# Optimization experiments

Measured on AMD Instinct MI355X. Metric: run time of the kernel, lower is better.

Reference implementation:

```python
import jax, jax.numpy as jnp
import numpy as np
import math

G, T, D, B = 20000, 1536, 512, 256
TOPK = 32


def setup_inputs() -> dict:
    key = jax.random.key(0)
    k1, k2, k3, k4 = jax.random.split(key, 4)
    tg_dec = jax.random.normal(k1, (G, D), dtype=jnp.float32)
    tf_base = jax.random.normal(k2, (T, D), dtype=jnp.float32)
    tf_expr = jax.random.normal(k3, (B, T), dtype=jnp.float32)
    motif_mask = jax.random.randint(k4, (G, T), 0, 2).astype(jnp.int32)
    scale = jnp.full((1,), 0.1, dtype=jnp.float32)  # nn.Parameter scale
    return {"tg_dec": tg_dec, "tf_base": tf_base, "tf_expr": tf_expr,
            "motif_mask": motif_mask, "scale": scale}


def reference(tg_dec, tf_base, tf_expr, motif_mask, scale):
    # scaled similarity: [G, T]
    sim = jnp.matmul(tg_dec, tf_base.T) / math.sqrt(tf_base.shape[1])
    # masked fill where motif prior is absent
    sim = jnp.where(motif_mask == 0, -jnp.inf, sim)
    attn = jax.nn.softmax(sim, axis=-1)
    attn = jnp.nan_to_num(attn, nan=0.0)
    # top-k selection + scatter mask + renormalize
    _, topk_idx = jax.lax.top_k(attn, TOPK)              # [G, TOPK]
    rows = jnp.arange(attn.shape[0])[:, None]
    mask = jnp.zeros_like(attn).at[rows, topk_idx].set(1.0)
    attn = attn * mask
    attn = attn / (attn.sum(axis=-1, keepdims=True) + 1e-8)
    # weighted combine: [B, G]
    tf_scalar = jnp.matmul(tf_expr, attn.T)
    # dropout is identity in eval mode
    return (scale[0] * tf_scalar, attn)
```

## Files before the change

### kernel.cpp

```cpp
#include <hip/hip_runtime.h>
#include <cstdint>

typedef unsigned short u16;
typedef unsigned int   u32;
typedef unsigned long long u64;

#define G_ROWS 20000
#define G_PAD  20096
#define T_DIM  1536
#define D_DIM  512
#define B_DIM  256
#define TOPK   32
#define SIM_SCALE 0.04419417382415922f
#define SQRT_D    22.62741699796952f
#define BOUND_EPS 2.0e-4f

typedef __bf16 bf16x8 __attribute__((ext_vector_type(8)));
typedef float  f32x4  __attribute__((ext_vector_type(4)));

__device__ __forceinline__ u16 f2bf(float f) {
  u32 u = __float_as_uint(f);
  u += 0x7fffu + ((u >> 16) & 1u);
  return (u16)(u >> 16);
}
__device__ __forceinline__ float bf2f(u16 h) {
  return __uint_as_float(((u32)h) << 16);
}
__device__ __forceinline__ u32 fkey(float v) {
  u32 b = __float_as_uint(v);
  return (b & 0x80000000u) ? ~b : (b | 0x80000000u);
}
__device__ __forceinline__ float funkey(u32 o) {
  u32 b = (o & 0x80000000u) ? (o & 0x7FFFFFFFu) : ~o;
  return __uint_as_float(b);
}

__global__ __launch_bounds__(256) void prep(const float* __restrict__ tg_dec,
                                            const float* __restrict__ tf_base,
                                            const float* __restrict__ tf_expr,
                                            u16* __restrict__ Ah, u16* __restrict__ Al,
                                            u16* __restrict__ Bh, u16* __restrict__ Bl,
                                            float* __restrict__ tfT)
{
  __shared__ float tile[32][33];
  const int b = blockIdx.x;
  const int tid = threadIdx.x;
  if (b < 10816) {
    const float* src; u16 *hi, *lo; int valid_rows; int bb;
    if (b < 10048) { src = tg_dec; hi = Ah; lo = Al; valid_rows = G_ROWS; bb = b; }
    else           { src = tf_base; hi = Bh; lo = Bl; valid_rows = T_DIM; bb = b - 10048; }
    size_t i = ((size_t)bb * 256 + tid) * 4;
    int row = (int)(i >> 9);
    float4 a = make_float4(0.f, 0.f, 0.f, 0.f);
    if (row < valid_rows) a = *(const float4*)(src + i);
    float v[4] = {a.x, a.y, a.z, a.w};
    u16 h[4], l[4];
#pragma unroll
    for (int c = 0; c < 4; ++c) {
      h[c] = f2bf(v[c]);
      l[c] = f2bf(v[c] - bf2f(h[c]));
    }
    *(uint2*)(hi + i) = make_uint2((u32)h[0] | ((u32)h[1] << 16), (u32)h[2] | ((u32)h[3] << 16));
    *(uint2*)(lo + i) = make_uint2((u32)l[0] | ((u32)l[1] << 16), (u32)l[2] | ((u32)l[3] << 16));
  } else {
    const int t = b - 10816;
    const int x = tid & 31, y = tid >> 5;
    const int bt = (t % 48) * 32;
    const int bb = (t / 48) * 32;
#pragma unroll
    for (int i = 0; i < 32; i += 8) tile[y + i][x] = tf_expr[(size_t)(bb + y + i) * T_DIM + bt + x];
    __syncthreads();
#pragma unroll
    for (int i = 0; i < 32; i += 8) tfT[(size_t)(bt + y + i) * B_DIM + bb + x] = tile[x][y + i];
  }
}

__device__ __forceinline__ void gl16(const u16* g, u16* l) {
  __builtin_amdgcn_global_load_lds((__attribute__((address_space(1))) void*)(void*)g,
                                   (__attribute__((address_space(3))) void*)l, 16, 0, 0);
}

#define NBX 6
#define NWG 474

__global__ __launch_bounds__(512, 2) void gemm_split(const u16* __restrict__ Ah, const u16* __restrict__ Al,
                                                     const u16* __restrict__ Bh, const u16* __restrict__ Bl,
                                                     float* __restrict__ Sim)
{
  __shared__ u16 sm[65536];

  const int orig = blockIdx.x;
  const int xcd  = orig & 7;
  const int q    = NWG >> 3, r = NWG & 7;
  const int wgid = (xcd < r ? xcd * (q + 1) : r * (q + 1) + (xcd - r) * q) + (orig >> 3);
  const int by   = wgid / NBX;
  const int bx   = wgid - by * NBX;
  const int bm0  = by * 256;
  const int bn0  = bx * 256;

  const int tid  = threadIdx.x;
  const int lane = tid & 63;
  const int wv   = tid >> 6;
  const int wm   = wv >> 2;
  const int wn   = wv & 3;
  const int la8  = lane << 3;

  const int sub  = wv << 1;
  const int srow = lane & 15;
  const int skc  = (lane >> 4) << 3;
  const u16* gA0 = Ah + (size_t)(bm0 + (sub + 0) * 16 + srow) * 512 + skc;
  const u16* gA1 = Ah + (size_t)(bm0 + (sub + 1) * 16 + srow) * 512 + skc;
  const u16* gAl0 = Al + (size_t)(bm0 + (sub + 0) * 16 + srow) * 512 + skc;
  const u16* gAl1 = Al + (size_t)(bm0 + (sub + 1) * 16 + srow) * 512 + skc;
  const u16* gB0 = Bh + (size_t)(bn0 + (sub + 0) * 16 + srow) * 512 + skc;
  const u16* gB1 = Bh + (size_t)(bn0 + (sub + 1) * 16 + srow) * 512 + skc;
  const u16* gBl0 = Bl + (size_t)(bn0 + (sub + 0) * 16 + srow) * 512 + skc;
  const u16* gBl1 = Bl + (size_t)(bn0 + (sub + 1) * 16 + srow) * 512 + skc;

#define STAGE_A(p, ktn) do {                                   \
    const size_t ko = (size_t)(ktn) << 5;                      \
    u16* d = sm + (p) * 16384 + sub * 512;                     \
    gl16(gA0 + ko,  d);                                        \
    gl16(gA1 + ko,  d + 512);                                  \
    gl16(gAl0 + ko, d + 8192);                                 \
    gl16(gAl1 + ko, d + 8192 + 512);                           \
  } while (0)
#define STAGE_B(p, ktn) do {                                   \
    const size_t ko = (size_t)(ktn) << 5;                      \
    u16* d = sm + 32768 + (p) * 16384 + sub * 512;             \
    gl16(gB0 + ko,  d);                                        \
    gl16(gB1 + ko,  d + 512);                                  \
    gl16(gBl0 + ko, d + 8192);                                 \
    gl16(gBl1 + ko, d + 8192 + 512);                           \
  } while (0)

  f32x4 acc[8][4];
#pragma unroll
  for (int i = 0; i < 8; ++i)
#pragma unroll
    for (int j = 0; j < 4; ++j) acc[i][j] = (f32x4){0.f, 0.f, 0.f, 0.f};

  bf16x8 aH[4], aL[4], bH[4], bL[4];

#define READ_A(rbA, half) do {                                                     \
    _Pragma("unroll")                                                              \
    for (int i = 0; i < 4; ++i) {                                                  \
      aH[i] = *(const bf16x8*)((rbA) + (wm * 8 + (half) * 4 + i) * 512 + la8);     \
      aL[i] = *(const bf16x8*)((rbA) + 8192 + (wm * 8 + (half) * 4 + i) * 512 + la8); \
    }                                                                              \
  } while (0)
#define READ_B(rbB, half) do {                                                     \
    _Pragma("unroll")                                                              \
    for (int i = 0; i < 2; ++i) {                                                  \
      bH[(half) * 2 + i] = *(const bf16x8*)((rbB) + (wn * 4 + (half) * 2 + i) * 512 + la8); \
      bL[(half) * 2 + i] = *(const bf16x8*)((rbB) + 8192 + (wn * 4 + (half) * 2 + i) * 512 + la8); \
    }                                                                              \
  } while (0)
#define MFMA_Q(qm, qn) do {                                                        \
    __builtin_amdgcn_s_setprio(1);                                                 \
    _Pragma("unroll")                                                              \
    for (int m2 = 0; m2 < 4; ++m2)                                                 \
      _Pragma("unroll")                                                            \
      for (int n2 = 0; n2 < 2; ++n2) {                                             \
        const int mi = (qm) * 4 + m2, ni = (qn) * 2 + n2;                          \
        acc[mi][ni] = __builtin_amdgcn_mfma_f32_16x16x32_bf16(aH[m2], bH[ni], acc[mi][ni], 0, 0, 0); \
        acc[mi][ni] = __builtin_amdgcn_mfma_f32_16x16x32_bf16(aH[m2], bL[ni], acc[mi][ni], 0, 0, 0); \
        acc[mi][ni] = __builtin_amdgcn_mfma_f32_16x16x32_bf16(aL[m2], bH[ni], acc[mi][ni], 0, 0, 0); \
      }                                                                            \
    __builtin_amdgcn_s_setprio(0);                                                 \
  } while (0)
#define LGKM0 do { asm volatile("s_waitcnt lgkmcnt(0)" ::: "memory"); __builtin_amdgcn_sched_barrier(0); } while (0)
#define BAR   do { __builtin_amdgcn_sched_barrier(0); __builtin_amdgcn_s_barrier(); } while (0)

  STAGE_A(0, 0);
  STAGE_B(0, 0);
  STAGE_A(1, 1);

#pragma unroll 2
  for (int kt = 0; kt < 16; ++kt) {
    const u16* rbA = sm + (kt & 1) * 16384;
    const u16* rbB = sm + 32768 + (kt & 1) * 16384;

    asm volatile("s_waitcnt vmcnt(4)" ::: "memory");
    BAR;
    READ_A(rbA, 0);
    READ_B(rbB, 0);
    LGKM0;
    MFMA_Q(0, 0);
    BAR;

    if (kt < 15) STAGE_B((kt + 1) & 1, kt + 1);
    READ_B(rbB, 1);
    LGKM0;
    MFMA_Q(0, 1);
    BAR;

    READ_A(rbA, 1);
    LGKM0;
    MFMA_Q(1, 0);
    BAR;

    if (kt < 14) STAGE_A(kt & 1, kt + 2);
    MFMA_Q(1, 1);
  }
#undef STAGE_A
#undef STAGE_B
#undef READ_A
#undef READ_B
#undef MFMA_Q
#undef LGKM0
#undef BAR

  const int erow0 = bm0 + (wm << 7) + ((lane >> 4) << 2);
  const int ecol0 = bn0 + (wn << 6) + (lane & 15);
#pragma unroll
  for (int mi = 0; mi < 8; ++mi)
#pragma unroll
    for (int rr = 0; rr < 4; ++rr) {
      int row = erow0 + mi * 16 + rr;
      if (row < G_ROWS) {
#pragma unroll
        for (int ni = 0; ni < 4; ++ni)
          Sim[(size_t)row * T_DIM + ecol0 + ni * 16] = acc[mi][ni][rr] * SIM_SCALE;
      }
    }
}

__device__ __forceinline__ int count_ge(const float* v, float tau) {
  int c = 0;
#pragma unroll
  for (int j = 0; j < 24; ++j) c += (int)__popcll(__ballot(v[j] >= tau));
  return c;
}
__device__ __forceinline__ u64 bitonic64_desc(u64 key, int lane) {
#pragma unroll
  for (int k = 2; k <= 64; k <<= 1) {
#pragma unroll
    for (int j = k >> 1; j > 0; j >>= 1) {
      u64 p = __shfl_xor(key, j, 64);
      bool lower = (lane & j) == 0;
      bool asc   = (lane & k) != 0;
      u64 mn = (key < p) ? key : p;
      u64 mx = (key < p) ? p : key;
      key = (lower == asc) ? mn : mx;
    }
  }
  return key;
}

__global__ __launch_bounds__(256) void topk_kernel(float* __restrict__ Sim, const int* __restrict__ mask,
                                                   const float* __restrict__ tg_dec,
                                                   const float* __restrict__ tf_base,
                                                   int* __restrict__ tIdx, float* __restrict__ tW)
{
  __shared__ u32 cval[4][64];
  __shared__ int cidxs[4][64];
  const int lane = threadIdx.x & 63;
  const int wv   = threadIdx.x >> 6;
  const int g    = blockIdx.x * 4 + wv;
  float* row = Sim + (size_t)g * T_DIM;
  const int* mrow = mask + (size_t)g * T_DIM;

  float v[24];
#pragma unroll
  for (int j = 0; j < 6; ++j) {
    float4 q = *(const float4*)(row + j * 256 + lane * 4);
    int4  mq = *(const int4*)(mrow + j * 256 + lane * 4);
    v[j * 4 + 0] = mq.x ? q.x : -INFINITY;
    v[j * 4 + 1] = mq.y ? q.y : -INFINITY;
    v[j * 4 + 2] = mq.z ? q.z : -INFINITY;
    v[j * 4 + 3] = mq.w ? q.w : -INFINITY;
  }

  const float TH0 = 1.25f, TH1 = 1.40f, TH2 = 1.55f, TH3 = 1.70f, TH4 = 1.85f, TH5 = 2.00f;
  int n0 = 0, n1 = 0, n2 = 0, n3 = 0, n4 = 0, n5 = 0, nv = 0;
#pragma unroll
  for (int j = 0; j < 24; ++j) {
    float x = v[j];
    n0 += (x >= TH0); n1 += (x >= TH1); n2 += (x >= TH2);
    n3 += (x >= TH3); n4 += (x >= TH4); n5 += (x >= TH5);
    nv += (x != -INFINITY);
  }
  u64 p0 = (u64)(u32)n0 | ((u64)(u32)n1 << 16) | ((u64)(u32)n2 << 32) | ((u64)(u32)n3 << 48);
  u64 p1 = (u64)(u32)n4 | ((u64)(u32)n5 << 16) | ((u64)(u32)nv << 32);
#pragma unroll
  for (int off = 32; off > 0; off >>= 1) {
    p0 += __shfl_xor(p0, off, 64);
    p1 += __shfl_xor(p1, off, 64);
  }
  int c[6];
  c[0] = (int)(p0 & 0xFFFF); c[1] = (int)((p0 >> 16) & 0xFFFF);
  c[2] = (int)((p0 >> 32) & 0xFFFF); c[3] = (int)((p0 >> 48) & 0xFFFF);
  c[4] = (int)(p1 & 0xFFFF); c[5] = (int)((p1 >> 16) & 0xFFFF);
  const int cvalid = (int)((p1 >> 32) & 0xFFFF);

  float tau; int cnt;
  if (cvalid <= 64) { tau = -3.0e38f; cnt = cvalid; }
  else {
    int is = -1;
#pragma unroll
    for (int i = 0; i < 6; ++i) if (c[i] >= 33) is = i;
    const float THv[7] = {TH0, TH1, TH2, TH3, TH4, TH5, 8.0f};
    if (is >= 0 && c[is] <= 64) { tau = THv[is]; cnt = c[is]; }
    else {
      float lo, hi;
      if (is < 0) { lo = -4.0f; hi = TH0; }
      else        { lo = THv[is]; hi = THv[is + 1]; }
      tau = lo; cnt = 1000;
      for (int it = 0; it < 16; ++it) {
        float mid = 0.5f * (lo + hi);
        int cm = count_ge(v, mid);
        if (cm > 64)      lo = mid;
        else if (cm < 33) hi = mid;
        else { tau = mid; cnt = cm; break; }
      }
      if (cnt == 1000) tau = lo;
    }
  }

  int base = 0;
#pragma unroll
  for (int j = 0; j < 24; ++j) {
    bool pred = (v[j] >= tau);
    u64 bmc = __ballot(pred);
    int pos = base + (int)__popcll(bmc & ((1ull << lane) - 1ull));
    int idx = (j >> 2) * 256 + lane * 4 + (j & 3);
    if (pred && pos < 64) { cval[wv][pos] = fkey(v[j]); cidxs[wv][pos] = idx; }
    base += (int)__popcll(bmc);
  }
  const int cnt_eff = (base < 64) ? base : 64;

  u64 key = 0;
  if (lane < cnt_eff)
    key = ((u64)cval[wv][lane] << 32) | (u64)(u32)(~(u32)cidxs[wv][lane]);

  key = bitonic64_desc(key, lane);
  int   myidx = (int)(~(u32)key);
  float myv   = (key != 0) ? funkey((u32)(key >> 32)) : -INFINITY;

  float v31 = __shfl(myv, 31, 64);
  float v32 = __shfl(myv, 32, 64);
  if (cnt_eff > TOPK && (v31 - v32) < 2.0f * BOUND_EPS) {
    bool flag = (lane < cnt_eff) &&
                (myv >= v32 - 2.0f * BOUND_EPS) && (myv <= v31 + 2.0f * BOUND_EPS);
    if (flag) {
      const float* arow_g = tg_dec + (size_t)g * D_DIM;
      const float* brow   = tf_base + (size_t)myidx * D_DIM;
      float s1 = 0.f, s2 = 0.f;
#pragma unroll 8
      for (int k = 0; k < 384; k += 4) {
        float4 av = *(const float4*)(arow_g + k);
        float4 bv = *(const float4*)(brow + k);
        s1 = fmaf(av.x, bv.x, s1); s1 = fmaf(av.y, bv.y, s1);
        s1 = fmaf(av.z, bv.z, s1); s1 = fmaf(av.w, bv.w, s1);
      }
#pragma unroll 8
      for (int k = 384; k < 512; k += 4) {
        float4 av = *(const float4*)(arow_g + k);
        float4 bv = *(const float4*)(brow + k);
        s2 = fmaf(av.x, bv.x, s2); s2 = fmaf(av.y, bv.y, s2);
        s2 = fmaf(av.z, bv.z, s2); s2 = fmaf(av.w, bv.w, s2);
      }
      myv = (s1 + s2) / SQRT_D;
      key = ((u64)fkey(myv) << 32) | (u64)(u32)(~(u32)myidx);
    }
    key = bitonic64_desc(key, lane);
    myidx = (int)(~(u32)key);
    myv   = (key != 0) ? funkey((u32)(key >> 32)) : -INFINITY;
  }

  const bool selme = (lane < TOPK) && (lane < cnt_eff);
  float mx = __shfl(myv, 0, 64);
  float e = selme ? __expf(myv - mx) : 0.f;
  float E = e;
#pragma unroll
  for (int off = 32; off > 0; off >>= 1) E += __shfl_xor(E, off, 64);
  float rden = (E > 0.f) ? (1.f / E) : 0.f;
  float w = e * rden;

  const float4 z4 = make_float4(0.f, 0.f, 0.f, 0.f);
#pragma unroll
  for (int j = 0; j < 6; ++j) *(float4*)(row + j * 256 + lane * 4) = z4;
  asm volatile("s_waitcnt vmcnt(0)" ::: "memory");
  if (selme) row[myidx] = w;

  if (cnt_eff < TOPK && lane >= cnt_eff && lane < TOPK) {
    tIdx[(size_t)g * TOPK + lane] = 0; tW[(size_t)g * TOPK + lane] = 0.f;
  }
  if (selme) {
    tIdx[(size_t)g * TOPK + lane] = myidx;
    tW[(size_t)g * TOPK + lane]   = w;
  }
}

__global__ __launch_bounds__(256) void combine_kernel(const float* __restrict__ tfT, const int* __restrict__ tIdx,
                                                      const float* __restrict__ tW, const float* __restrict__ scalep,
                                                      float* __restrict__ out0)
{
  __shared__ int   sIdx[16 * 32];
  __shared__ float sW[16 * 32];
  const int tid = threadIdx.x;
  const int g0 = blockIdx.x * 16;
  for (int i = tid; i < 512; i += 256) {
    sIdx[i] = tIdx[(size_t)g0 * 32 + i];
    sW[i]   = tW[(size_t)g0 * 32 + i];
  }
  __syncthreads();
  const float scale = scalep[0];
  float acc[16];
#pragma unroll
  for (int gi = 0; gi < 16; ++gi) acc[gi] = 0.f;
#pragma unroll 4
  for (int gi = 0; gi < 16; ++gi) {
    float a = 0.f;
#pragma unroll
    for (int k = 0; k < 32; ++k) {
      float w = sW[gi * 32 + k];
      int t   = sIdx[gi * 32 + k];
      a += w * tfT[(size_t)t * B_DIM + tid];
    }
    acc[gi] = a;
  }
  float* dst = out0 + (size_t)tid * G_ROWS + g0;
#pragma unroll
  for (int q = 0; q < 4; ++q) {
    float4 o = make_float4(scale * acc[4*q], scale * acc[4*q+1], scale * acc[4*q+2], scale * acc[4*q+3]);
    *(float4*)(dst + 4 * q) = o;
  }
}

extern "C" void kernel_launch(void* const* d_in, const int* in_sizes, int n_in,
                              void* d_out, int out_size, void* d_ws, size_t ws_size,
                              hipStream_t stream)
{
  const float* tg_dec     = (const float*)d_in[0];
  const float* tf_base    = (const float*)d_in[1];
  const float* tf_expr    = (const float*)d_in[2];
  const int*   motif_mask = (const int*)d_in[3];
  const float* scale      = (const float*)d_in[4];

  float* out0 = (float*)d_out;
  float* attn = out0 + (size_t)B_DIM * G_ROWS;

  char* ws = (char*)d_ws;
  u16*   Ah    = (u16*)(ws);
  u16*   Al    = (u16*)(ws + 20578304);
  u16*   Bh    = (u16*)(ws + 41156608);
  u16*   Bl    = (u16*)(ws + 42729472);
  float* tfT   = (float*)(ws + 44302336);
  int*   tIdx  = (int*)(ws + 45875200);
  float* tW    = (float*)(ws + 48435200);

  prep<<<11200, 256, 0, stream>>>(tg_dec, tf_base, tf_expr, Ah, Al, Bh, Bl, tfT);
  gemm_split<<<NWG, 512, 0, stream>>>(Ah, Al, Bh, Bl, attn);
  topk_kernel<<<5000, 256, 0, stream>>>(attn, motif_mask, tg_dec, tf_base, tIdx, tW);
  combine_kernel<<<1250, 256, 0, stream>>>(tfT, tIdx, tW, scale, out0);
}
```

Measured before the change: 425.0 us.

## Fuse weighted combine into top-k kernel and drain loads on last GEMM step

The combine stage now runs inside the top-k kernel: each wave gathers tfT rows by its selected indices via shuffles and writes output columns through shared memory. This removes a separate kernel launch and the global round trip of the top-k indices and weights. Output stores now cover only 4 consecutive g per row instead of 16, which may reduce write coalescing. The GEMM's final k-iteration also waits for all outstanding loads rather than leaving four in flight.

```diff
diff --git a/kernel.cpp b/kernel.cpp
--- a/kernel.cpp
+++ b/kernel.cpp
@@ -108,12 +108,12 @@
   const int sub  = wv << 1;
   const int srow = lane & 15;
   const int skc  = (lane >> 4) << 3;
-  const u16* gA0 = Ah + (size_t)(bm0 + (sub + 0) * 16 + srow) * 512 + skc;
-  const u16* gA1 = Ah + (size_t)(bm0 + (sub + 1) * 16 + srow) * 512 + skc;
+  const u16* gA0  = Ah + (size_t)(bm0 + (sub + 0) * 16 + srow) * 512 + skc;
+  const u16* gA1  = Ah + (size_t)(bm0 + (sub + 1) * 16 + srow) * 512 + skc;
   const u16* gAl0 = Al + (size_t)(bm0 + (sub + 0) * 16 + srow) * 512 + skc;
   const u16* gAl1 = Al + (size_t)(bm0 + (sub + 1) * 16 + srow) * 512 + skc;
-  const u16* gB0 = Bh + (size_t)(bn0 + (sub + 0) * 16 + srow) * 512 + skc;
-  const u16* gB1 = Bh + (size_t)(bn0 + (sub + 1) * 16 + srow) * 512 + skc;
+  const u16* gB0  = Bh + (size_t)(bn0 + (sub + 0) * 16 + srow) * 512 + skc;
+  const u16* gB1  = Bh + (size_t)(bn0 + (sub + 1) * 16 + srow) * 512 + skc;
   const u16* gBl0 = Bl + (size_t)(bn0 + (sub + 0) * 16 + srow) * 512 + skc;
   const u16* gBl1 = Bl + (size_t)(bn0 + (sub + 1) * 16 + srow) * 512 + skc;
 
@@ -181,7 +181,8 @@
     const u16* rbA = sm + (kt & 1) * 16384;
     const u16* rbB = sm + 32768 + (kt & 1) * 16384;
 
-    asm volatile("s_waitcnt vmcnt(4)" ::: "memory");
+    if (kt < 15) asm volatile("s_waitcnt vmcnt(4)" ::: "memory");
+    else         asm volatile("s_waitcnt vmcnt(0)" ::: "memory");
     BAR;
     READ_A(rbA, 0);
     READ_B(rbB, 0);
@@ -248,13 +249,16 @@
   return key;
 }
 
-__global__ __launch_bounds__(256) void topk_kernel(float* __restrict__ Sim, const int* __restrict__ mask,
-                                                   const float* __restrict__ tg_dec,
-                                                   const float* __restrict__ tf_base,
-                                                   int* __restrict__ tIdx, float* __restrict__ tW)
+__global__ __launch_bounds__(256) void topk_combine(float* __restrict__ Sim, const int* __restrict__ mask,
+                                                    const float* __restrict__ tg_dec,
+                                                    const float* __restrict__ tf_base,
+                                                    const float* __restrict__ tfT,
+                                                    const float* __restrict__ scalep,
+                                                    float* __restrict__ out0)
 {
   __shared__ u32 cval[4][64];
   __shared__ int cidxs[4][64];
+  __shared__ float sOut[4][256];
   const int lane = threadIdx.x & 63;
   const int wv   = threadIdx.x >> 6;
   const int g    = blockIdx.x * 4 + wv;
@@ -345,19 +349,19 @@
                 (myv >= v32 - 2.0f * BOUND_EPS) && (myv <= v31 + 2.0f * BOUND_EPS);
     if (flag) {
       const float* arow_g = tg_dec + (size_t)g * D_DIM;
-      const float* brow   = tf_base + (size_t)myidx * D_DIM;
+      const float* brow2  = tf_base + (size_t)myidx * D_DIM;
       float s1 = 0.f, s2 = 0.f;
 #pragma unroll 8
       for (int k = 0; k < 384; k += 4) {
         float4 av = *(const float4*)(arow_g + k);
-        float4 bv = *(const float4*)(brow + k);
+        float4 bv = *(const float4*)(brow2 + k);
         s1 = fmaf(av.x, bv.x, s1); s1 = fmaf(av.y, bv.y, s1);
         s1 = fmaf(av.z, bv.z, s1); s1 = fmaf(av.w, bv.w, s1);
       }
 #pragma unroll 8
       for (int k = 384; k < 512; k += 4) {
         float4 av = *(const float4*)(arow_g + k);
-        float4 bv = *(const float4*)(brow + k);
+        float4 bv = *(const float4*)(brow2 + k);
         s2 = fmaf(av.x, bv.x, s2); s2 = fmaf(av.y, bv.y, s2);
         s2 = fmaf(av.z, bv.z, s2); s2 = fmaf(av.w, bv.w, s2);
       }
@@ -381,52 +385,30 @@
   const float4 z4 = make_float4(0.f, 0.f, 0.f, 0.f);
 #pragma unroll
   for (int j = 0; j < 6; ++j) *(float4*)(row + j * 256 + lane * 4) = z4;
+
+  float a0 = 0.f, a1 = 0.f, a2 = 0.f, a3 = 0.f;
+#pragma unroll 4
+  for (int k = 0; k < TOPK; ++k) {
+    float wk = __shfl(w, k, 64);
+    int   ik = __shfl(myidx, k, 64);
+    if (wk > 0.f) {
+      float4 vv = *(const float4*)(tfT + (size_t)ik * B_DIM + lane * 4);
+      a0 = fmaf(wk, vv.x, a0); a1 = fmaf(wk, vv.y, a1);
+      a2 = fmaf(wk, vv.z, a2); a3 = fmaf(wk, vv.w, a3);
+    }
+  }
+  const float scale = scalep[0];
+  *(float4*)(&sOut[wv][lane * 4]) = make_float4(scale * a0, scale * a1, scale * a2, scale * a3);
+  __syncthreads();
+  {
+    const int t = threadIdx.x;
+    const int g0 = blockIdx.x * 4;
+    float4 o = make_float4(sOut[0][t], sOut[1][t], sOut[2][t], sOut[3][t]);
+    *(float4*)(out0 + (size_t)t * G_ROWS + g0) = o;
+  }
+
   asm volatile("s_waitcnt vmcnt(0)" ::: "memory");
   if (selme) row[myidx] = w;
-
-  if (cnt_eff < TOPK && lane >= cnt_eff && lane < TOPK) {
-    tIdx[(size_t)g * TOPK + lane] = 0; tW[(size_t)g * TOPK + lane] = 0.f;
-  }
-  if (selme) {
-    tIdx[(size_t)g * TOPK + lane] = myidx;
-    tW[(size_t)g * TOPK + lane]   = w;
-  }
-}
-
-__global__ __launch_bounds__(256) void combine_kernel(const float* __restrict__ tfT, const int* __restrict__ tIdx,
-                                                      const float* __restrict__ tW, const float* __restrict__ scalep,
-                                                      float* __restrict__ out0)
-{
-  __shared__ int   sIdx[16 * 32];
-  __shared__ float sW[16 * 32];
-  const int tid = threadIdx.x;
-  const int g0 = blockIdx.x * 16;
-  for (int i = tid; i < 512; i += 256) {
-    sIdx[i] = tIdx[(size_t)g0 * 32 + i];
-    sW[i]   = tW[(size_t)g0 * 32 + i];
-  }
-  __syncthreads();
-  const float scale = scalep[0];
-  float acc[16];
-#pragma unroll
-  for (int gi = 0; gi < 16; ++gi) acc[gi] = 0.f;
-#pragma unroll 4
-  for (int gi = 0; gi < 16; ++gi) {
-    float a = 0.f;
-#pragma unroll
-    for (int k = 0; k < 32; ++k) {
-      float w = sW[gi * 32 + k];
-      int t   = sIdx[gi * 32 + k];
-      a += w * tfT[(size_t)t * B_DIM + tid];
-    }
-    acc[gi] = a;
-  }
-  float* dst = out0 + (size_t)tid * G_ROWS + g0;
-#pragma unroll
-  for (int q = 0; q < 4; ++q) {
-    float4 o = make_float4(scale * acc[4*q], scale * acc[4*q+1], scale * acc[4*q+2], scale * acc[4*q+3]);
-    *(float4*)(dst + 4 * q) = o;
-  }
 }
 
 extern "C" void kernel_launch(void* const* d_in, const int* in_sizes, int n_in,
@@ -448,11 +430,8 @@
   u16*   Bh    = (u16*)(ws + 41156608);
   u16*   Bl    = (u16*)(ws + 42729472);
   float* tfT   = (float*)(ws + 44302336);
-  int*   tIdx  = (int*)(ws + 45875200);
-  float* tW    = (float*)(ws + 48435200);
 
   prep<<<11200, 256, 0, stream>>>(tg_dec, tf_base, tf_expr, Ah, Al, Bh, Bl, tfT);
   gemm_split<<<NWG, 512, 0, stream>>>(Ah, Al, Bh, Bl, attn);
-  topk_kernel<<<5000, 256, 0, stream>>>(attn, motif_mask, tg_dec, tf_base, tIdx, tW);
-  combine_kernel<<<1250, 256, 0, stream>>>(tfT, tIdx, tW, scale, out0);
-}
+  topk_combine<<<5000, 256, 0, stream>>>(attn, motif_mask, tg_dec, tf_base, tfT, scale, out0);
+}
```

New measurement: 430.5 us. Within noise of the previous version (+1.3%).
